# Kernel optimization log

Hardware: AMD Instinct MI355X
Metric: run time of the kernel (lower is better)

Reference implementation:

```python
import jax, jax.numpy as jnp
import numpy as np

N = 100000   # nodes
DEG = 4      # fixed out-degree (>2 so every node survives the c>2 mask)
E = N * DEG  # edges
IN = 128
H = 256


def _lin_params(key, fan_out, fan_in, bias=True):
    k1, k2 = jax.random.split(key)
    W = 0.05 * jax.random.normal(k1, (fan_out, fan_in), jnp.float32)
    if bias:
        b = 0.05 * jax.random.normal(k2, (fan_out,), jnp.float32)
        return W, b
    return W


def setup_inputs() -> dict:
    key = jax.random.key(0)
    ks = jax.random.split(key, 12)
    x = jax.random.normal(ks[0], (N, IN), jnp.float32)
    # every node has exactly DEG outgoing edges -> out-degree 4 > 2 for all nodes
    src = jnp.repeat(jnp.arange(N, dtype=jnp.int32), DEG)
    dst = jax.random.randint(ks[1], (E,), 0, N, dtype=jnp.int32)
    edge_index = jnp.stack([src, dst])  # [2, E]
    batch = jnp.zeros((N,), jnp.int32)
    Wr0, br0 = _lin_params(ks[2], H, IN)
    Ws0 = _lin_params(ks[3], H, IN, bias=False)
    Wr1, br1 = _lin_params(ks[4], H, H)
    Ws1 = _lin_params(ks[5], H, H, bias=False)
    Wr2, br2 = _lin_params(ks[6], H, H)
    Ws2 = _lin_params(ks[7], H, H, bias=False)
    Wsp1, bsp1 = _lin_params(ks[8], 1, H)
    Wsp2, bsp2 = _lin_params(ks[9], 1, H)
    Wl, bl = _lin_params(ks[10], 1, 2)
    return dict(x=x, edge_index=edge_index, batch=batch,
                Wr0=Wr0, br0=br0, Ws0=Ws0,
                Wr1=Wr1, br1=br1, Ws1=Ws1,
                Wr2=Wr2, br2=br2, Ws2=Ws2,
                Wsp1=Wsp1, bsp1=bsp1, Wsp2=Wsp2, bsp2=bsp2,
                Wl=Wl, bl=bl)


def reference(x, edge_index, batch, Wr0, br0, Ws0, Wr1, br1, Ws1,
              Wr2, br2, Ws2, Wsp1, bsp1, Wsp2, bsp2, Wl, bl):
    src, dst = edge_index[0], edge_index[1]

    def gconv(h, Wr, br, Ws):
        # PyG GraphConv(aggr='add'): out_i = W_rel @ sum_{j->i} h_j + b + W_root @ h_i
        agg = jax.ops.segment_sum(h[src], dst, num_segments=N)
        return jax.nn.relu(agg @ Wr.T + br + h @ Ws.T)

    h = gconv(x, Wr0, br0, Ws0)
    h = gconv(h, Wr1, br1, Ws1)
    h = gconv(h, Wr2, br2, Ws2)

    # unique(edge_index[0], counts) ; keep source nodes with out-degree > 2
    deg = jax.ops.segment_sum(jnp.ones((E,), h.dtype), src, num_segments=N)
    sel = jnp.nonzero(deg > 2, size=N, fill_value=0)[0]  # all N nodes by construction
    xs = h[sel].reshape(-1, 2 * H)  # pair consecutive nodes
    x1, x2 = xs[:, :H], xs[:, H:]
    out = jnp.concatenate([jax.nn.relu(x1 @ Wsp1.T + bsp1),
                           jax.nn.relu(x2 @ Wsp2.T + bsp2)], axis=1)
    y = jax.nn.sigmoid(out @ Wl.T + bl)  # split=True branch
    return y, xs, x1, x2
```

## Files before the change

### kernel.cpp

```cpp
#include <hip/hip_runtime.h>
#include <hip/hip_bf16.h>
#include <math.h>

#define NNODES 100000
#define NEDGES 400000
#define INDIM  128
#define HDIM   256
#define MAXDEG 32

#define BM 64
#define BN 256
#define BK 64
#define MTILES 1563

typedef __attribute__((ext_vector_type(8))) short short8;
typedef __attribute__((ext_vector_type(8))) unsigned short ushort8v;
typedef __attribute__((ext_vector_type(4))) float f32x4;

__device__ __forceinline__ float bf2f(unsigned short u) {
    union { unsigned int i; float f; } v; v.i = ((unsigned int)u) << 16; return v.f;
}
__device__ __forceinline__ unsigned short f2bf(float f) {
    union { float f; unsigned int i; } v; v.f = f;
    unsigned int r = v.i + 0x7fffu + ((v.i >> 16) & 1u);
    return (unsigned short)(r >> 16);
}

#define XB_BLOCKS 12500
#define W0_BLOCKS 256
#define W1_BLOCKS 512
#define EL_BLOCKS 1563
#define PREP_BLOCKS (XB_BLOCKS + W0_BLOCKS + 2 * W1_BLOCKS + EL_BLOCKS)

__global__ void prep_kernel(const float* __restrict__ x, unsigned short* __restrict__ xb,
                            const float* __restrict__ Wr0, const float* __restrict__ Ws0,
                            unsigned short* __restrict__ B0,
                            const float* __restrict__ Wr1, const float* __restrict__ Ws1,
                            unsigned short* __restrict__ B1,
                            const float* __restrict__ Wr2, const float* __restrict__ Ws2,
                            unsigned short* __restrict__ B2,
                            const int* __restrict__ ei, int* __restrict__ cnt,
                            int* __restrict__ elist) {
    int b = blockIdx.x;
    if (b < XB_BLOCKS) {
        int i = b * 256 + threadIdx.x;
        float4 v = ((const float4*)x)[i];
        ushort4 o; o.x = f2bf(v.x); o.y = f2bf(v.y); o.z = f2bf(v.z); o.w = f2bf(v.w);
        ((ushort4*)xb)[i] = o;
        return;
    }
    b -= XB_BLOCKS;
    if (b < W0_BLOCKS + 2 * W1_BLOCKS) {
        const float *Wr, *Ws; unsigned short* B; int K;
        if (b < W0_BLOCKS)               { Wr = Wr0; Ws = Ws0; B = B0; K = INDIM; }
        else if (b < W0_BLOCKS + W1_BLOCKS) { Wr = Wr1; Ws = Ws1; B = B1; K = HDIM; b -= W0_BLOCKS; }
        else                              { Wr = Wr2; Ws = Ws2; B = B2; K = HDIM; b -= W0_BLOCKS + W1_BLOCKS; }
        int idx = b * 256 + threadIdx.x;
        int n = idx / (2 * K);
        int k = idx - n * 2 * K;
        float v = (k < K) ? Wr[n * K + k] : Ws[n * K + (k - K)];
        B[idx] = f2bf(v);
        return;
    }
    b -= W0_BLOCKS + 2 * W1_BLOCKS;
    int e = b * 256 + threadIdx.x;
    if (e < NEDGES) {
        int d = ei[NEDGES + e];
        int s = ei[e];
        int pos = atomicAdd(&cnt[d], 1);
        if (pos < MAXDEG) elist[d * MAXDEG + pos] = s;
    }
}

template<int MODE, int K>
__global__ __launch_bounds__(256, 3)
void fused_gconv(const unsigned short* __restrict__ h,
                 const int* __restrict__ cnt, const int* __restrict__ elist,
                 const unsigned short* __restrict__ B, const float* __restrict__ bias,
                 unsigned short* __restrict__ hout,
                 float* __restrict__ xs, float* __restrict__ x1o, float* __restrict__ x2o,
                 const float* __restrict__ Wsp1, const float* __restrict__ Wsp2,
                 float* __restrict__ spart) {
    __shared__ __align__(16) unsigned char smem[32768];
    unsigned short* Agg = (unsigned short*)smem;

    const int tid  = threadIdx.x;
    const int lane = tid & 63;
    const int wv   = tid >> 6;
    const int m0   = blockIdx.x * BM;
    constexpr int Ktot = 2 * K;

    const int lane31 = lane & 31;
    const int hw     = lane >> 5;
    int pn = m0 + wv * 16 + (lane >> 2);
    if (pn >= NNODES) pn = NNODES - 1;
    const int4 elv = ((const int4*)(elist + (size_t)pn * MAXDEG))[lane & 3];
    int cnode = m0 + wv * 16 + (lane & 15);
    if (cnode >= NNODES) cnode = NNODES - 1;
    const int cv = cnt[cnode];

    if constexpr (K == 256) {
        for (int rd = 0; rd < 8; rd++) {
            const int iw = rd * 2 + hw;
            int cA = __shfl(cv, rd * 2);
            int cB = __shfl(cv, rd * 2 + 1);
            if (cA > MAXDEG) cA = MAXDEG;
            if (cB > MAXDEG) cB = MAXDEG;
            const int c    = hw ? cB : cA;
            const int cmax = cA > cB ? cA : cB;
            int node = m0 + wv * 16 + iw;
            if (node >= NNODES) node = NNODES - 1;
            float a[8];
            #pragma unroll
            for (int i = 0; i < 8; i++) a[i] = 0.f;
            for (int j0 = 0; j0 < cmax; j0 += 4) {
                int4 e;
                if (j0 < 16) {
                    int src = iw * 4 + (j0 >> 2);
                    e.x = __shfl(elv.x, src); e.y = __shfl(elv.y, src);
                    e.z = __shfl(elv.z, src); e.w = __shfl(elv.w, src);
                } else {
                    e = ((const int4*)(elist + (size_t)node * MAXDEG))[j0 >> 2];
                }
                int rem = c - j0;
                ushort8v v0 = {0,0,0,0,0,0,0,0}, v1 = v0, v2 = v0, v3 = v0;
                if (rem > 0) v0 = ((const ushort8v*)(h + (size_t)e.x * 256))[lane31];
                if (rem > 1) v1 = ((const ushort8v*)(h + (size_t)e.y * 256))[lane31];
                if (rem > 2) v2 = ((const ushort8v*)(h + (size_t)e.z * 256))[lane31];
                if (rem > 3) v3 = ((const ushort8v*)(h + (size_t)e.w * 256))[lane31];
                #pragma unroll
                for (int i = 0; i < 8; i++)
                    a[i] += bf2f(v0[i]) + bf2f(v1[i]) + bf2f(v2[i]) + bf2f(v3[i]);
            }
            int r = wv * 16 + iw;
            int sgp = (lane31 & ~7) | ((lane31 ^ r) & 7);
            ushort8v o;
            #pragma unroll
            for (int i = 0; i < 8; i++) o[i] = f2bf(a[i]);
            *(ushort8v*)&Agg[r * 256 + sgp * 8] = o;
        }
    } else {
        for (int rd = 0; rd < 8; rd++) {
            const int iw = rd * 2 + hw;
            int cA = __shfl(cv, rd * 2);
            int cB = __shfl(cv, rd * 2 + 1);
            if (cA > MAXDEG) cA = MAXDEG;
            if (cB > MAXDEG) cB = MAXDEG;
            const int c    = hw ? cB : cA;
            const int cmax = cA > cB ? cA : cB;
            int node = m0 + wv * 16 + iw;
            if (node >= NNODES) node = NNODES - 1;
            float a0 = 0.f, a1 = 0.f, a2 = 0.f, a3 = 0.f;
            for (int j0 = 0; j0 < cmax; j0 += 4) {
                int4 e;
                if (j0 < 16) {
                    int src = iw * 4 + (j0 >> 2);
                    e.x = __shfl(elv.x, src); e.y = __shfl(elv.y, src);
                    e.z = __shfl(elv.z, src); e.w = __shfl(elv.w, src);
                } else {
                    e = ((const int4*)(elist + (size_t)node * MAXDEG))[j0 >> 2];
                }
                int rem = c - j0;
                ushort4 v0 = {0,0,0,0}, v1 = {0,0,0,0}, v2 = {0,0,0,0}, v3 = {0,0,0,0};
                if (rem > 0) v0 = ((const ushort4*)(h + (size_t)e.x * 128))[lane31];
                if (rem > 1) v1 = ((const ushort4*)(h + (size_t)e.y * 128))[lane31];
                if (rem > 2) v2 = ((const ushort4*)(h + (size_t)e.z * 128))[lane31];
                if (rem > 3) v3 = ((const ushort4*)(h + (size_t)e.w * 128))[lane31];
                a0 += bf2f(v0.x) + bf2f(v1.x) + bf2f(v2.x) + bf2f(v3.x);
                a1 += bf2f(v0.y) + bf2f(v1.y) + bf2f(v2.y) + bf2f(v3.y);
                a2 += bf2f(v0.z) + bf2f(v1.z) + bf2f(v2.z) + bf2f(v3.z);
                a3 += bf2f(v0.w) + bf2f(v1.w) + bf2f(v2.w) + bf2f(v3.w);
            }
            int r = wv * 16 + iw;
            int sg = lane31 >> 1;
            int sgp = (sg & ~7) | ((sg ^ r) & 7);
            ushort4 o; o.x = f2bf(a0); o.y = f2bf(a1); o.z = f2bf(a2); o.w = f2bf(a3);
            *(ushort4*)&Agg[r * 128 + sgp * 8 + (lane31 & 1) * 4] = o;
        }
    }

    f32x4 acc[4][4];
    #pragma unroll
    for (int i = 0; i < 4; i++)
        #pragma unroll
        for (int j = 0; j < 4; j++)
            acc[i][j] = (f32x4){0.f, 0.f, 0.f, 0.f};

    const int l15  = lane & 15;
    const int seg0 = lane >> 4;

    #pragma unroll
    for (int k0 = 0; k0 < K; k0 += BK) {
        #pragma unroll
        for (int half = 0; half < 2; half++) {
            const int seg = half * 4 + seg0;
            short8 af[4], bfr[4];
            #pragma unroll
            for (int mt = 0; mt < 4; mt++) {
                int grow = m0 + mt * 16 + l15; if (grow >= NNODES) grow = NNODES - 1;
                af[mt] = *(const short8*)(h + (size_t)grow * K + k0 + seg * 8);
            }
            #pragma unroll
            for (int nt = 0; nt < 4; nt++) {
                int nl = wv * 64 + nt * 16 + l15;
                bfr[nt] = *(const short8*)(B + (size_t)nl * Ktot + K + k0 + seg * 8);
            }
            #pragma unroll
            for (int mt = 0; mt < 4; mt++)
                #pragma unroll
                for (int nt = 0; nt < 4; nt++)
                    acc[mt][nt] = __builtin_amdgcn_mfma_f32_16x16x32_bf16(
                        af[mt], bfr[nt], acc[mt][nt], 0, 0, 0);
        }
    }

    __syncthreads();

    #pragma unroll
    for (int k0 = 0; k0 < K; k0 += BK) {
        #pragma unroll
        for (int half = 0; half < 2; half++) {
            const int seg = half * 4 + seg0;
            short8 af[4], bfr[4];
            #pragma unroll
            for (int nt = 0; nt < 4; nt++) {
                int nl = wv * 64 + nt * 16 + l15;
                bfr[nt] = *(const short8*)(B + (size_t)nl * Ktot + k0 + seg * 8);
            }
            #pragma unroll
            for (int mt = 0; mt < 4; mt++) {
                int ml = mt * 16 + l15;
                int sg = (k0 >> 3) + seg;
                int sgp = (sg & ~7) | ((sg ^ ml) & 7);
                af[mt] = *(const short8*)&Agg[ml * K + sgp * 8];
            }
            #pragma unroll
            for (int mt = 0; mt < 4; mt++)
                #pragma unroll
                for (int nt = 0; nt < 4; nt++)
                    acc[mt][nt] = __builtin_amdgcn_mfma_f32_16x16x32_bf16(
                        af[mt], bfr[nt], acc[mt][nt], 0, 0, 0);
        }
    }

    float* bounce = (float*)smem;
    float* wb = bounce + wv * (16 * 68);
    const int q    = lane & 3;
    const int rrow = lane >> 2;

    #pragma unroll
    for (int mt = 0; mt < 4; mt++) {
        __syncthreads();
        #pragma unroll
        for (int nt = 0; nt < 4; nt++)
            #pragma unroll
            for (int rr = 0; rr < 4; rr++)
                wb[((lane >> 4) * 4 + rr) * 68 + nt * 16 + (lane & 15)] = acc[mt][nt][rr];
        __syncthreads();

        int grow = m0 + mt * 16 + rrow;
        int gc   = wv * 64 + q * 16;
        float4 v[4];
        #pragma unroll
        for (int s = 0; s < 4; s++)
            v[s] = ((const float4*)(wb + rrow * 68 + q * 16))[s];

        if (grow < NNODES) {
            const float4* bv = (const float4*)(bias + gc);
            #pragma unroll
            for (int s = 0; s < 4; s++) {
                float4 b4 = bv[s];
                v[s].x = fmaxf(v[s].x + b4.x, 0.f);
                v[s].y = fmaxf(v[s].y + b4.y, 0.f);
                v[s].z = fmaxf(v[s].z + b4.z, 0.f);
                v[s].w = fmaxf(v[s].w + b4.w, 0.f);
            }
            if (MODE == 0) {
                ushort8v o0, o1;
                o0[0]=f2bf(v[0].x); o0[1]=f2bf(v[0].y); o0[2]=f2bf(v[0].z); o0[3]=f2bf(v[0].w);
                o0[4]=f2bf(v[1].x); o0[5]=f2bf(v[1].y); o0[6]=f2bf(v[1].z); o0[7]=f2bf(v[1].w);
                o1[0]=f2bf(v[2].x); o1[1]=f2bf(v[2].y); o1[2]=f2bf(v[2].z); o1[3]=f2bf(v[2].w);
                o1[4]=f2bf(v[3].x); o1[5]=f2bf(v[3].y); o1[6]=f2bf(v[3].z); o1[7]=f2bf(v[3].w);
                ushort8v* dst = (ushort8v*)(hout + (size_t)grow * HDIM + gc);
                dst[0] = o0; dst[1] = o1;
            } else {
                float4* xsp = (float4*)(xs + (size_t)grow * HDIM + gc);
                #pragma unroll
                for (int s = 0; s < 4; s++) xsp[s] = v[s];
                float* xo = (grow & 1) ? x2o : x1o;
                float4* xop = (float4*)(xo + (size_t)(grow >> 1) * HDIM + gc);
                #pragma unroll
                for (int s = 0; s < 4; s++) xop[s] = v[s];
                const float* wsp = (grow & 1) ? Wsp2 : Wsp1;
                const float4* wv4 = (const float4*)(wsp + gc);
                float p = 0.f;
                #pragma unroll
                for (int s = 0; s < 4; s++) {
                    float4 w4 = wv4[s];
                    p += v[s].x * w4.x + v[s].y * w4.y + v[s].z * w4.z + v[s].w * w4.w;
                }
                p += __shfl_xor(p, 1);
                p += __shfl_xor(p, 2);
                if (q == 0) atomicAdd(&spart[grow], p);
            }
        }
    }
}

__global__ void finalize_kernel(const float* __restrict__ spart, const float* __restrict__ bsp1,
                                const float* __restrict__ bsp2, const float* __restrict__ Wl,
                                const float* __restrict__ bl, float* __restrict__ y) {
    int p = blockIdx.x * 256 + threadIdx.x;
    if (p < NNODES / 2) {
        float s1 = spart[2 * p]     + bsp1[0]; s1 = s1 > 0.f ? s1 : 0.f;
        float s2 = spart[2 * p + 1] + bsp2[0]; s2 = s2 > 0.f ? s2 : 0.f;
        float t = s1 * Wl[0] + s2 * Wl[1] + bl[0];
        y[p] = 1.f / (1.f + expf(-t));
    }
}

extern "C" void kernel_launch(void* const* d_in, const int* in_sizes, int n_in,
                              void* d_out, int out_size, void* d_ws, size_t ws_size,
                              hipStream_t stream) {
    const float* x    = (const float*)d_in[0];
    const int*   ei   = (const int*)d_in[1];
    const float* Wr0  = (const float*)d_in[3];
    const float* br0  = (const float*)d_in[4];
    const float* Ws0  = (const float*)d_in[5];
    const float* Wr1  = (const float*)d_in[6];
    const float* br1  = (const float*)d_in[7];
    const float* Ws1  = (const float*)d_in[8];
    const float* Wr2  = (const float*)d_in[9];
    const float* br2  = (const float*)d_in[10];
    const float* Ws2  = (const float*)d_in[11];
    const float* Wsp1 = (const float*)d_in[12];
    const float* bsp1 = (const float*)d_in[13];
    const float* Wsp2 = (const float*)d_in[14];
    const float* bsp2 = (const float*)d_in[15];
    const float* Wl   = (const float*)d_in[16];
    const float* bl   = (const float*)d_in[17];

    char* ws = (char*)d_ws;
    size_t off = 0;
    auto alloc = [&](size_t bytes) -> void* {
        void* p = ws + off;
        off += (bytes + 255) & ~(size_t)255;
        return p;
    };
    int*            cnt   = (int*)alloc((size_t)NNODES * 4);
    float*          spart = (float*)alloc((size_t)NNODES * 4);
    size_t zero_bytes = off;
    int*            elist = (int*)alloc((size_t)NNODES * MAXDEG * 4);
    unsigned short* xb    = (unsigned short*)alloc((size_t)NNODES * INDIM * 2);
    unsigned short* hA    = (unsigned short*)alloc((size_t)NNODES * HDIM * 2);
    unsigned short* hB    = (unsigned short*)alloc((size_t)NNODES * HDIM * 2);
    unsigned short* B0    = (unsigned short*)alloc((size_t)HDIM * 2 * INDIM * 2);
    unsigned short* B1    = (unsigned short*)alloc((size_t)HDIM * 2 * HDIM * 2);
    unsigned short* B2    = (unsigned short*)alloc((size_t)HDIM * 2 * HDIM * 2);

    float* y  = (float*)d_out;
    float* xs = y + 50000;
    float* x1 = xs + (size_t)50000 * 512;
    float* x2 = x1 + (size_t)50000 * 256;

    hipMemsetAsync(ws, 0, zero_bytes, stream);
    prep_kernel<<<PREP_BLOCKS, 256, 0, stream>>>(x, xb, Wr0, Ws0, B0, Wr1, Ws1, B1,
                                                 Wr2, Ws2, B2, ei, cnt, elist);

    fused_gconv<0, 128><<<MTILES, 256, 0, stream>>>(xb, cnt, elist, B0, br0, hA,
                                                    nullptr, nullptr, nullptr,
                                                    nullptr, nullptr, nullptr);
    fused_gconv<0, 256><<<MTILES, 256, 0, stream>>>(hA, cnt, elist, B1, br1, hB,
                                                    nullptr, nullptr, nullptr,
                                                    nullptr, nullptr, nullptr);
    fused_gconv<1, 256><<<MTILES, 256, 0, stream>>>(hB, cnt, elist, B2, br2, nullptr,
                                                    xs, x1, x2, Wsp1, Wsp2, spart);
    finalize_kernel<<<(NNODES / 2 + 255) / 256, 256, 0, stream>>>(
        spart, bsp1, bsp2, Wl, bl, y);
}
```

Before: 666.7 us.

## Prefetch root features into LDS asynchronously during aggregation and merge GEMM loops

The kernel now starts asynchronous global-to-LDS loads (global_load_lds) of the block's root-node feature tile before the neighbour gather, so the self-term operand arrives while aggregation runs, instead of being read from global memory inside the GEMM loop. The two separate GEMM passes (root weights and relation weights) are merged into one loop that reads both A operands from swizzled LDS. Shared memory doubles, and launch bounds drop from 3 to 2 blocks per CU, which trades occupancy for the overlap and lower global-memory latency in the MFMA loop.

Result: faster. 625.9 us (-6.1%).

```diff
diff --git a/kernel.cpp b/kernel.cpp
--- a/kernel.cpp
+++ b/kernel.cpp
@@ -10,7 +10,6 @@
 
 #define BM 64
 #define BN 256
-#define BK 64
 #define MTILES 1563
 
 typedef __attribute__((ext_vector_type(8))) short short8;
@@ -24,6 +23,13 @@
     union { float f; unsigned int i; } v; v.f = f;
     unsigned int r = v.i + 0x7fffu + ((v.i >> 16) & 1u);
     return (unsigned short)(r >> 16);
+}
+
+__device__ __forceinline__ void async_load16(const void* g, void* l) {
+    __builtin_amdgcn_global_load_lds(
+        (const __attribute__((address_space(1))) unsigned int*)g,
+        (__attribute__((address_space(3))) unsigned int*)l,
+        16, 0, 0);
 }
 
 #define XB_BLOCKS 12500
@@ -73,7 +79,7 @@
 }
 
 template<int MODE, int K>
-__global__ __launch_bounds__(256, 3)
+__global__ __launch_bounds__(256, 2)
 void fused_gconv(const unsigned short* __restrict__ h,
                  const int* __restrict__ cnt, const int* __restrict__ elist,
                  const unsigned short* __restrict__ B, const float* __restrict__ bias,
@@ -81,14 +87,16 @@
                  float* __restrict__ xs, float* __restrict__ x1o, float* __restrict__ x2o,
                  const float* __restrict__ Wsp1, const float* __restrict__ Wsp2,
                  float* __restrict__ spart) {
-    __shared__ __align__(16) unsigned char smem[32768];
-    unsigned short* Agg = (unsigned short*)smem;
+    __shared__ __align__(16) unsigned char smem[64 * K * 2 * 2];
+    unsigned short* Agg  = (unsigned short*)smem;
+    unsigned short* A2sh = (unsigned short*)(smem + 64 * K * 2);
 
     const int tid  = threadIdx.x;
     const int lane = tid & 63;
     const int wv   = tid >> 6;
     const int m0   = blockIdx.x * BM;
     constexpr int Ktot = 2 * K;
+    constexpr int SEGS = K / 8;
 
     const int lane31 = lane & 31;
     const int hw     = lane >> 5;
@@ -98,6 +106,15 @@
     int cnode = m0 + wv * 16 + (lane & 15);
     if (cnode >= NNODES) cnode = NNODES - 1;
     const int cv = cnt[cnode];
+
+    #pragma unroll
+    for (int it = 0; it < (64 * SEGS) / 256; it++) {
+        int idx = it * 256 + tid;
+        int row = idx / SEGS, seg = idx % SEGS;
+        int gseg = (seg & ~7) | ((seg ^ (row & 7)) & 7);
+        int grow = m0 + row; if (grow >= NNODES) grow = NNODES - 1;
+        async_load16(h + (size_t)grow * K + gseg * 8, &A2sh[idx * 8]);
+    }
 
     if constexpr (K == 256) {
         for (int rd = 0; rd < 8; rd++) {
@@ -179,6 +196,8 @@
         }
     }
 
+    __syncthreads();
+
     f32x4 acc[4][4];
     #pragma unroll
     for (int i = 0; i < 4; i++)
@@ -190,56 +209,36 @@
     const int seg0 = lane >> 4;
 
     #pragma unroll
-    for (int k0 = 0; k0 < K; k0 += BK) {
+    for (int k0 = 0; k0 < K; k0 += 64) {
         #pragma unroll
         for (int half = 0; half < 2; half++) {
-            const int seg = half * 4 + seg0;
-            short8 af[4], bfr[4];
-            #pragma unroll
-            for (int mt = 0; mt < 4; mt++) {
-                int grow = m0 + mt * 16 + l15; if (grow >= NNODES) grow = NNODES - 1;
-                af[mt] = *(const short8*)(h + (size_t)grow * K + k0 + seg * 8);
-            }
+            const int sg = (k0 >> 3) + half * 4 + seg0;
+            short8 afr[4], afs[4], bwr[4], bws[4];
             #pragma unroll
             for (int nt = 0; nt < 4; nt++) {
                 int nl = wv * 64 + nt * 16 + l15;
-                bfr[nt] = *(const short8*)(B + (size_t)nl * Ktot + K + k0 + seg * 8);
+                bwr[nt] = *(const short8*)(B + (size_t)nl * Ktot + sg * 8);
+                bws[nt] = *(const short8*)(B + (size_t)nl * Ktot + K + sg * 8);
+            }
+            #pragma unroll
+            for (int mt = 0; mt < 4; mt++) {
+                int ml  = mt * 16 + l15;
+                int sgp = (sg & ~7) | ((sg ^ ml) & 7);
+                afr[mt] = *(const short8*)&Agg [ml * K + sgp * 8];
+                afs[mt] = *(const short8*)&A2sh[ml * K + sgp * 8];
             }
             #pragma unroll
             for (int mt = 0; mt < 4; mt++)
                 #pragma unroll
                 for (int nt = 0; nt < 4; nt++)
                     acc[mt][nt] = __builtin_amdgcn_mfma_f32_16x16x32_bf16(
-                        af[mt], bfr[nt], acc[mt][nt], 0, 0, 0);
-        }
-    }
-
-    __syncthreads();
-
-    #pragma unroll
-    for (int k0 = 0; k0 < K; k0 += BK) {
-        #pragma unroll
-        for (int half = 0; half < 2; half++) {
-            const int seg = half * 4 + seg0;
-            short8 af[4], bfr[4];
-            #pragma unroll
-            for (int nt = 0; nt < 4; nt++) {
-                int nl = wv * 64 + nt * 16 + l15;
-                bfr[nt] = *(const short8*)(B + (size_t)nl * Ktot + k0 + seg * 8);
-            }
-            #pragma unroll
-            for (int mt = 0; mt < 4; mt++) {
-                int ml = mt * 16 + l15;
-                int sg = (k0 >> 3) + seg;
-                int sgp = (sg & ~7) | ((sg ^ ml) & 7);
-                af[mt] = *(const short8*)&Agg[ml * K + sgp * 8];
-            }
+                        afr[mt], bwr[nt], acc[mt][nt], 0, 0, 0);
             #pragma unroll
             for (int mt = 0; mt < 4; mt++)
                 #pragma unroll
                 for (int nt = 0; nt < 4; nt++)
                     acc[mt][nt] = __builtin_amdgcn_mfma_f32_16x16x32_bf16(
-                        af[mt], bfr[nt], acc[mt][nt], 0, 0, 0);
+                        afs[mt], bws[nt], acc[mt][nt], 0, 0, 0);
         }
     }
 
```
